# Kernel optimization log

Hardware: AMD Instinct MI355X
Metric: run time of the kernel (lower is better)

The kernel has to match this reference:

```python
import jax, jax.numpy as jnp
import numpy as np

DIM = 384
HEADS = 12
WS = (2, 7, 7)
SS = (1, 3, 3)
B, D, H, W = 4, 8, 56, 56
N = WS[0] * WS[1] * WS[2]  # 98


def _win_part_np(x, ws):
    b, d, h, w, c = x.shape
    x = x.reshape(b, d // ws[0], ws[0], h // ws[1], ws[1], w // ws[2], ws[2], c)
    return x.transpose(0, 1, 3, 5, 2, 4, 6, 7).reshape(-1, ws[0] * ws[1] * ws[2], c)


def setup_inputs() -> dict:
    key = jax.random.key(0)
    ks = jax.random.split(key, 6)
    s = 0.02
    x = jax.random.normal(ks[0], (B, D, H, W, DIM), jnp.float32)
    # relative position index (static int buffer)
    coords = np.stack(np.meshgrid(np.arange(WS[0]), np.arange(WS[1]), np.arange(WS[2]), indexing='ij')).reshape(3, -1)
    rel = (coords[:, :, None] - coords[:, None, :]).transpose(1, 2, 0)
    rel[..., 0] += WS[0] - 1
    rel[..., 1] += WS[1] - 1
    rel[..., 2] += WS[2] - 1
    rel[..., 0] *= (2 * WS[1] - 1) * (2 * WS[2] - 1)
    rel[..., 1] *= 2 * WS[2] - 1
    rel_index = jnp.asarray(rel.sum(-1), jnp.int32)  # [N, N]
    # shifted-window attention mask (standard Swin construction)
    img = np.zeros((1, D, H, W, 1), np.float32)
    cnt = 0
    for dsl in (slice(0, -WS[0]), slice(-WS[0], -SS[0]), slice(-SS[0], None)):
        for hsl in (slice(0, -WS[1]), slice(-WS[1], -SS[1]), slice(-SS[1], None)):
            for wsl in (slice(0, -WS[2]), slice(-WS[2], -SS[2]), slice(-SS[2], None)):
                img[:, dsl, hsl, wsl, :] = cnt
                cnt += 1
    mw = _win_part_np(img, WS).squeeze(-1)  # [nW, N]
    attn_mask = np.where(mw[:, None, :] != mw[:, :, None], -100.0, 0.0).astype(np.float32)
    table_size = (2 * WS[0] - 1) * (2 * WS[1] - 1) * (2 * WS[2] - 1)
    return {
        'x': x,
        'mask': jnp.asarray(attn_mask),
        'rel_table': jax.random.normal(ks[1], (table_size, HEADS), jnp.float32) * s,
        'rel_index': rel_index,
        'qkv_w': jax.random.normal(ks[2], (3 * DIM, DIM), jnp.float32) * s,
        'qkv_b': jnp.zeros((3 * DIM,), jnp.float32),
        'proj_w': jax.random.normal(ks[3], (DIM, DIM), jnp.float32) * s,
        'proj_b': jnp.zeros((DIM,), jnp.float32),
        'g1': jnp.ones((DIM,), jnp.float32), 'b1': jnp.zeros((DIM,), jnp.float32),
        'g2': jnp.ones((DIM,), jnp.float32), 'b2': jnp.zeros((DIM,), jnp.float32),
        'fc1_w': jax.random.normal(ks[4], (DIM, DIM), jnp.float32) * s,
        'fc1_b': jnp.zeros((DIM,), jnp.float32),
        'fc2_w': jax.random.normal(ks[5], (DIM, DIM), jnp.float32) * s,
        'fc2_b': jnp.zeros((DIM,), jnp.float32),
    }


def _ln(x, g, b, eps=1e-5):
    mu = x.mean(-1, keepdims=True)
    var = jnp.mean((x - mu) ** 2, axis=-1, keepdims=True)
    return (x - mu) * jax.lax.rsqrt(var + eps) * g + b


def _window_partition(x, ws):
    b, d, h, w, c = x.shape
    x = x.reshape(b, d // ws[0], ws[0], h // ws[1], ws[1], w // ws[2], ws[2], c)
    return x.transpose(0, 1, 3, 5, 2, 4, 6, 7).reshape(-1, ws[0] * ws[1] * ws[2], c)


def _window_reverse(win, ws, b, d, h, w):
    x = win.reshape(b, d // ws[0], h // ws[1], w // ws[2], ws[0], ws[1], ws[2], -1)
    return x.transpose(0, 1, 4, 2, 5, 3, 6, 7).reshape(b, d, h, w, -1)


def reference(x, mask, rel_table, rel_index, qkv_w, qkv_b, proj_w, proj_b,
              g1, b1, g2, b2, fc1_w, fc1_b, fc2_w, fc2_b):
    shortcut = x
    h = _ln(x, g1, b1)
    b, d, hh, ww, c = h.shape
    # get_window_size: clamp window/shift to input extents (static here)
    ws = [min(WS[i], (d, hh, ww)[i]) for i in range(3)]
    ss = [0 if (d, hh, ww)[i] <= WS[i] else SS[i] for i in range(3)]
    pad = [(ws[i] - (d, hh, ww)[i] % ws[i]) % ws[i] for i in range(3)]
    h = jnp.pad(h, ((0, 0), (0, pad[0]), (0, pad[1]), (0, pad[2]), (0, 0)))
    dp, hp, wp = h.shape[1:4]
    if any(ss):
        h = jnp.roll(h, shift=(-ss[0], -ss[1], -ss[2]), axis=(1, 2, 3))
    xw = _window_partition(h, ws)  # [B_, N, C]
    bw, n, _ = xw.shape
    hd = c // HEADS
    qkv = (xw @ qkv_w.T + qkv_b).reshape(bw, n, 3, HEADS, hd).transpose(2, 0, 3, 1, 4)
    q, k, v = qkv[0], qkv[1], qkv[2]  # [B_, H, N, hd]
    scale = hd ** -0.5
    attn = jnp.einsum('bhnd,bhmd->bhnm', q * scale, k)
    bias = rel_table[rel_index[:n, :n].reshape(-1)].reshape(n, n, HEADS).transpose(2, 0, 1)
    attn = attn + bias[None]
    nW = mask.shape[0]
    attn = attn.reshape(bw // nW, nW, HEADS, n, n) + mask[None, :, None]
    attn = jax.nn.softmax(attn.reshape(bw, HEADS, n, n), axis=-1)
    out = jnp.einsum('bhnm,bhmd->bhnd', attn, v).transpose(0, 2, 1, 3).reshape(bw, n, c)
    out = out @ proj_w.T + proj_b
    out = _window_reverse(out, ws, b, dp, hp, wp)
    if any(ss):
        out = jnp.roll(out, shift=(ss[0], ss[1], ss[2]), axis=(1, 2, 3))
    out = out[:, :d, :hh, :ww, :]
    x1 = shortcut + out
    h2 = _ln(x1, g2, b2)
    mlp = jax.nn.gelu(h2 @ fc1_w.T + fc1_b, approximate=False) @ fc2_w.T + fc2_b
    return x1 + mlp
```

## Files before the change

### kernel.cpp

```cpp
#include <hip/hip_runtime.h>
#include <hip/hip_bf16.h>

#define HEADS 12
#define NWIN 1024
#define NW_MASK 256
#define NTOK 98
#define CDIM 384
#define NROWS (NWIN * NTOK)
#define QKVN (3 * CDIM)
#define PSTR 136
#define LOG2E 1.4426950408889634f
#define SCALE_LOG2E 0.25503486f
#define KSTEPS 12

using u16 = unsigned short;
typedef __attribute__((ext_vector_type(8))) short short8;
typedef __attribute__((ext_vector_type(4))) short s16x4;
typedef __attribute__((ext_vector_type(4))) float f32x4;
typedef __attribute__((ext_vector_type(2))) unsigned u32x2;

__device__ __forceinline__ float b2f(u16 u) { return __uint_as_float(((unsigned)u) << 16); }
__device__ __forceinline__ u16 f2b(float f) {
  unsigned u = __float_as_uint(f);
  u += 0x7FFF + ((u >> 16) & 1);
  return (u16)(u >> 16);
}

__device__ __forceinline__ int tok_of_row(int r) {
  int win = r / NTOK;
  int j   = r - win * NTOK;
  int b   = win >> 8;
  int wl  = win & 255;
  int wd = wl >> 6, wh = (wl >> 3) & 7, ww = wl & 7;
  int od = j / 49; int rem = j - od * 49;
  int oh = rem / 7; int ow = rem - oh * 7;
  int sd = (wd * 2 + od + 1) & 7;
  int sh = wh * 7 + oh + 3; if (sh >= 56) sh -= 56;
  int sw = ww * 7 + ow + 3; if (sw >= 56) sw -= 56;
  return ((b * 8 + sd) * 56 + sh) * 56 + sw;
}

__device__ __forceinline__ int xcd_swz(int bid, int nwg) {
  int q = nwg >> 3, r = nwg & 7;
  int xcd = bid & 7, i = bid >> 3;
  return ((xcd < r) ? xcd * (q + 1) : r * (q + 1) + (xcd - r) * q) + i;
}

__global__ void detect_kernel(const unsigned* __restrict__ g1w, int* __restrict__ flag) {
  if (threadIdx.x == 0 && blockIdx.x == 0)
    flag[0] = (g1w[0] == 0x3F800000u) ? 1 : 0;
}

__device__ __forceinline__ float raw_at(const void* src, size_t j, int isf32) {
  return isf32 ? ((const float*)src)[j] : b2f(((const u16*)src)[j]);
}

struct CvtArgs {
  const void* src[12];
  unsigned off[13];
};
__global__ __launch_bounds__(256) void cvt_all(CvtArgs a, u16* __restrict__ dst,
                                               const int* __restrict__ flag) {
  int i = blockIdx.x * 256 + threadIdx.x;
  if (i >= (int)a.off[12]) return;
  int s = 0;
#pragma unroll
  for (int k = 1; k < 12; ++k) s += (i >= (int)a.off[k]);
  int j = i - (int)a.off[s];
  dst[i] = flag[0] ? f2b(((const float*)a.src[s])[j]) : ((const u16*)a.src[s])[j];
}

template<bool GATHER>
__global__ __launch_bounds__(256) void ln_kernel(const void* __restrict__ in,
                                                 const u16* __restrict__ gam,
                                                 const u16* __restrict__ bet,
                                                 u16* __restrict__ outp,
                                                 const int* __restrict__ flag,
                                                 int maybe_f32) {
  int wrow = blockIdx.x * 4 + (threadIdx.x >> 6);
  int lane = threadIdx.x & 63;
  int isf32 = maybe_f32 ? flag[0] : 0;
  size_t srow = GATHER ? (size_t)tok_of_row(wrow) : (size_t)wrow;
  const u16*   ip16 = (const u16*)in + srow * CDIM;
  const float* ip32 = (const float*)in + srow * CDIM;
  float xv[6]; float s = 0.f, s2 = 0.f;
#pragma unroll
  for (int i = 0; i < 6; ++i) {
    int c = lane + 64 * i;
    xv[i] = isf32 ? ip32[c] : b2f(ip16[c]);
    s += xv[i]; s2 += xv[i] * xv[i];
  }
#pragma unroll
  for (int off = 1; off < 64; off <<= 1) {
    s  += __shfl_xor(s, off);
    s2 += __shfl_xor(s2, off);
  }
  float mu = s * (1.f / CDIM);
  float var = s2 * (1.f / CDIM) - mu * mu;
  float rstd = rsqrtf(var + 1e-5f);
  u16* op = outp + (size_t)wrow * CDIM;
#pragma unroll
  for (int i = 0; i < 6; ++i) {
    int c = lane + 64 * i;
    op[c] = f2b((xv[i] - mu) * rstd * b2f(gam[c]) + b2f(bet[c]));
  }
}

__global__ void bias_kernel(const void* __restrict__ tab, const int* __restrict__ idx,
                            float* __restrict__ biasf, const int* __restrict__ flag) {
  int i = blockIdx.x * 256 + threadIdx.x;
  if (i >= HEADS * NTOK * 100) return;
  int isf32 = flag[0];
  int h = i / (NTOK * 100);
  int rem = i - h * (NTOK * 100);
  int q = rem / 100, t = rem - q * 100;
  biasf[i] = (t < NTOK) ? raw_at(tab, (size_t)idx[q * NTOK + t] * HEADS + h, isf32) * LOG2E : 0.f;
}

__global__ void maskp_kernel(const void* __restrict__ msrc, u16* __restrict__ mdst,
                             const int* __restrict__ flag) {
  int i = blockIdx.x * 256 + threadIdx.x;
  if (i >= NW_MASK * NTOK * 100) return;
  int isf32 = flag[0];
  int w = i / (NTOK * 100);
  int rem = i - w * (NTOK * 100);
  int q = rem / 100, t = rem - q * 100;
  mdst[i] = (t < NTOK) ? f2b(raw_at(msrc, (size_t)(w * NTOK + q) * NTOK + t, isf32) * LOG2E)
                       : (u16)0;
}

__device__ __forceinline__ void gload16(const u16* g, u16* l) {
  __builtin_amdgcn_global_load_lds((const __attribute__((address_space(1))) unsigned*)g,
                                   (__attribute__((address_space(3))) unsigned*)l,
                                   16, 0, 0);
}

template<int EPI>
__global__ __launch_bounds__(256) void gemm_bt(const u16* __restrict__ A, int lda,
                                               const u16* __restrict__ W,
                                               const u16* __restrict__ bias,
                                               int NB, void* __restrict__ outb, int ldo,
                                               const void* __restrict__ aux,
                                               const int* __restrict__ flag) {
  __shared__ __align__(16) u16 lA[2][128 * 32];
  __shared__ __align__(16) u16 lB[2][128 * 32];
  int bid = xcd_swz(blockIdx.x, gridDim.x);
  int mb = bid / NB, nb = bid - mb * NB;
  int row0 = mb * 128, col0 = nb * 128;
  int tid = threadIdx.x;
  int lane = tid & 63;
  int wid = tid >> 6;
  int wr = (wid >> 1) * 64, wc = (wid & 1) * 64;
  f32x4 zero = {0.f, 0.f, 0.f, 0.f};
  f32x4 acc[4][4];
#pragma unroll
  for (int m = 0; m < 4; ++m)
#pragma unroll
    for (int n = 0; n < 4; ++n) acc[m][n] = zero;

  int r0 = tid >> 2, s0 = tid & 3;
  int r1 = 64 + r0;
  int c0 = 8 * (s0 ^ ((r0 >> 1) & 3));
  int c1 = 8 * (s0 ^ ((r1 >> 1) & 3));
  const u16* Ab0 = &A[(size_t)(row0 + r0) * lda + c0];
  const u16* Ab1 = &A[(size_t)(row0 + r1) * lda + c1];
  const u16* Wb0 = &W[(size_t)(col0 + r0) * CDIM + c0];
  const u16* Wb1 = &W[(size_t)(col0 + r1) * CDIM + c1];
  int e0 = tid * 8, e1 = 2048 + tid * 8;
  int g = (lane >> 4) * 8, fr = lane & 15;
  int sw = 8 * ((lane >> 4) ^ ((fr >> 1) & 3));

  gload16(Ab0, &lA[0][e0]);
  gload16(Ab1, &lA[0][e1]);
  gload16(Wb0, &lB[0][e0]);
  gload16(Wb1, &lB[0][e1]);
  __syncthreads();

#pragma unroll
  for (int t = 0; t < KSTEPS; ++t) {
    int cur = t & 1;
    if (t < KSTEPS - 1) {
      int kt = (t + 1) * 32;
      gload16(Ab0 + kt, &lA[cur ^ 1][e0]);
      gload16(Ab1 + kt, &lA[cur ^ 1][e1]);
      gload16(Wb0 + kt, &lB[cur ^ 1][e0]);
      gload16(Wb1 + kt, &lB[cur ^ 1][e1]);
    }
    short8 af[4], bf[4];
#pragma unroll
    for (int m = 0; m < 4; ++m) af[m] = *(const short8*)&lA[cur][(wr + m * 16 + fr) * 32 + sw];
#pragma unroll
    for (int n = 0; n < 4; ++n) bf[n] = *(const short8*)&lB[cur][(wc + n * 16 + fr) * 32 + sw];
#pragma unroll
    for (int m = 0; m < 4; ++m)
#pragma unroll
      for (int n = 0; n < 4; ++n)
        acc[m][n] = __builtin_amdgcn_mfma_f32_16x16x32_bf16(af[m], bf[n], acc[m][n], 0, 0, 0);
    __syncthreads();
  }

  int isf32 = (EPI == 1 || EPI == 3) ? flag[0] : 0;
  int colo = lane & 15;
  int rowo = (lane >> 4) * 4;
  float bv[4];
#pragma unroll
  for (int n = 0; n < 4; ++n) bv[n] = b2f(bias[col0 + wc + n * 16 + colo]);
#pragma unroll
  for (int m = 0; m < 4; ++m) {
#pragma unroll
    for (int r = 0; r < 4; ++r) {
      int gr = row0 + wr + m * 16 + rowo + r;
      int t = (EPI == 1 || EPI == 3) ? tok_of_row(gr) : 0;
#pragma unroll
      for (int n = 0; n < 4; ++n) {
        int gc = col0 + wc + n * 16 + colo;
        float v = acc[m][n][r] + bv[n];
        if (EPI == 0) {
          ((u16*)outb)[(size_t)gr * ldo + gc] = f2b(v);
        } else if (EPI == 1) {
          float xs = isf32 ? ((const float*)aux)[(size_t)t * CDIM + gc]
                           : b2f(((const u16*)aux)[(size_t)t * CDIM + gc]);
          ((u16*)outb)[(size_t)gr * ldo + gc] = f2b(v + xs);
        } else if (EPI == 2) {
          float ge = 0.5f * v * (1.f + erff(v * 0.70710678118654752f));
          ((u16*)outb)[(size_t)gr * ldo + gc] = f2b(ge);
        } else {
          float x1v = b2f(((const u16*)aux)[(size_t)gr * CDIM + gc]);
          float o = v + x1v;
          if (isf32) ((float*)outb)[(size_t)t * CDIM + gc] = o;
          else       ((u16*)outb)[(size_t)t * CDIM + gc] = f2b(o);
        }
      }
    }
  }
}

__global__ __launch_bounds__(256, 3) void attn_mfma(u16* __restrict__ qkv,
                                                    const u16* __restrict__ maskp,
                                                    const float* __restrict__ biasf) {
  __shared__ __align__(16) u16 P4[4][16 * PSTR];
  int wid = threadIdx.x >> 6, lane = threadIdx.x & 63;
  int gh = blockIdx.x * 4 + wid;
  int win = gh / HEADS, hd = gh - win * HEADS;
  int l15 = lane & 15, g = lane >> 4;
  u16* P = P4[wid];
  const size_t base = (size_t)win * NTOK * QKVN + (size_t)hd * 32;
  u16* qp = qkv + base;
  const u16* kp = qkv + base + CDIM;
  const u16* vp = qkv + base + 2 * CDIM;
  const f32x4 zero = {0.f, 0.f, 0.f, 0.f};

  { u32x2 z = {0u, 0u}; *(u32x2*)&P[l15 * PSTR + 112 + 4 * g] = z; }

  short8 kf[7];
#pragma unroll
  for (int n = 0; n < 7; ++n) {
    int tok = n * 16 + l15; if (tok > NTOK - 1) tok = NTOK - 1;
    kf[n] = *(const short8*)&kp[(size_t)tok * QKVN + 8 * g];
  }
  short8 vf[2][4];
#pragma unroll
  for (int kk = 0; kk < 4; ++kk)
#pragma unroll
    for (int i = 0; i < 8; ++i) {
      int tok = 32 * kk + 8 * g + i;
      const u16* vr = vp + (size_t)tok * QKVN + l15;
      u16 v0 = (tok < NTOK) ? vr[0]  : (u16)0;
      u16 v1 = (tok < NTOK) ? vr[16] : (u16)0;
      vf[0][kk][i] = (short)v0;
      vf[1][kk][i] = (short)v1;
    }

  const float* brow = biasf + (size_t)hd * NTOK * 100;
  const u16*   mrow = maskp + (size_t)(win & (NW_MASK - 1)) * NTOK * 100;

  for (int m = 0; m < 7; ++m) {
    int qrow = m * 16 + l15;
    int qr = qrow > NTOK - 1 ? NTOK - 1 : qrow;
    short8 qf = *(const short8*)&qp[(size_t)qr * QKVN + 8 * g];
    f32x4 st[7];
#pragma unroll
    for (int n = 0; n < 7; ++n)
      st[n] = __builtin_amdgcn_mfma_f32_16x16x32_bf16(kf[n], qf, zero, 0, 0, 0);

    float pv[7][4];
    float mx = -1e30f;
#pragma unroll
    for (int n = 0; n < 7; ++n) {
      f32x4 bb = *(const f32x4*)&brow[(size_t)qr * 100 + n * 16 + 4 * g];
      s16x4 mm = *(const s16x4*)&mrow[(size_t)qr * 100 + n * 16 + 4 * g];
#pragma unroll
      for (int r = 0; r < 4; ++r) {
        int tok = n * 16 + 4 * g + r;
        float s = st[n][r] * SCALE_LOG2E + bb[r] + b2f((u16)mm[r]);
        if (tok > NTOK - 1) s = -1e30f;
        pv[n][r] = s;
        mx = fmaxf(mx, s);
      }
    }
    mx = fmaxf(mx, __shfl_xor(mx, 16));
    mx = fmaxf(mx, __shfl_xor(mx, 32));
    float sum = 0.f;
#pragma unroll
    for (int n = 0; n < 7; ++n)
#pragma unroll
      for (int r = 0; r < 4; ++r) {
        float e = exp2f(pv[n][r] - mx);
        pv[n][r] = e; sum += e;
      }
    sum += __shfl_xor(sum, 16);
    sum += __shfl_xor(sum, 32);
    float inv = 1.f / sum;
#pragma unroll
    for (int n = 0; n < 7; ++n) {
      __hip_bfloat162 h0 = __float22bfloat162_rn(make_float2(pv[n][0] * inv, pv[n][1] * inv));
      __hip_bfloat162 h1 = __float22bfloat162_rn(make_float2(pv[n][2] * inv, pv[n][3] * inv));
      u32x2 wv = { *(unsigned*)&h0, *(unsigned*)&h1 };
      *(u32x2*)&P[l15 * PSTR + n * 16 + 4 * g] = wv;
    }
    f32x4 oa0 = zero, oa1 = zero;
#pragma unroll
    for (int kk = 0; kk < 4; ++kk) {
      short8 pf = *(const short8*)&P[l15 * PSTR + kk * 32 + 8 * g];
      oa0 = __builtin_amdgcn_mfma_f32_16x16x32_bf16(pf, vf[0][kk], oa0, 0, 0, 0);
      oa1 = __builtin_amdgcn_mfma_f32_16x16x32_bf16(pf, vf[1][kk], oa1, 0, 0, 0);
    }
#pragma unroll
    for (int r = 0; r < 4; ++r) {
      int row = m * 16 + 4 * g + r;
      if (row < NTOK) {
        qp[(size_t)row * QKVN + l15]      = f2b(oa0[r]);
        qp[(size_t)row * QKVN + 16 + l15] = f2b(oa1[r]);
      }
    }
  }
}

extern "C" void kernel_launch(void* const* d_in, const int* in_sizes, int n_in,
                              void* d_out, int out_size, void* d_ws, size_t ws_size,
                              hipStream_t stream) {
  (void)n_in; (void)out_size; (void)ws_size;
  const void* x    = d_in[0];
  const int* ridx  = (const int*)d_in[3];

  char* ws = (char*)d_ws;
  const size_t SZ_QKV = (size_t)NROWS * QKVN * 2;
  const size_t SZ_MAT = (size_t)NROWS * CDIM * 2;
  const size_t SZ_BIAS = (size_t)HEADS * NTOK * 100 * 4;
  const size_t SZ_MASKP = (size_t)NW_MASK * NTOK * 100 * 2;
  u16* qkv     = (u16*)ws;
  u16* bufA    = (u16*)(ws + SZ_QKV);
  u16* bufX1   = (u16*)(ws + SZ_QKV + SZ_MAT);
  float* biasf = (float*)(ws + SZ_QKV + 2 * SZ_MAT);
  u16* maskp   = (u16*)(ws + SZ_QKV + 2 * SZ_MAT + SZ_BIAS);
  int* flag    = (int*)(ws + SZ_QKV + 2 * SZ_MAT + SZ_BIAS + SZ_MASKP);
  u16* cvt     = (u16*)((char*)flag + 256);

  detect_kernel<<<1, 64, 0, stream>>>((const unsigned*)d_in[8], flag);

  CvtArgs ca;
  unsigned off = 0;
  u16* cp[16];
  for (int k = 0; k < 12; ++k) {
    int i = 4 + k;
    ca.src[k] = d_in[i];
    ca.off[k] = off;
    cp[i] = cvt + off;
    off += (unsigned)in_sizes[i];
  }
  ca.off[12] = off;
  cvt_all<<<(off + 255) / 256, 256, 0, stream>>>(ca, cvt, flag);

  bias_kernel<<<(HEADS * NTOK * 100 + 255) / 256, 256, 0, stream>>>(d_in[2], ridx, biasf, flag);
  maskp_kernel<<<(NW_MASK * NTOK * 100 + 255) / 256, 256, 0, stream>>>(d_in[1], maskp, flag);
  ln_kernel<true><<<NROWS / 4, 256, 0, stream>>>(x, cp[8], cp[9], bufA, flag, 1);
  gemm_bt<0><<<(NROWS / 128) * (QKVN / 128), 256, 0, stream>>>(
      bufA, CDIM, cp[4], cp[5], QKVN / 128, qkv, QKVN, nullptr, flag);
  attn_mfma<<<(NWIN * HEADS) / 4, 256, 0, stream>>>(qkv, maskp, biasf);
  gemm_bt<1><<<(NROWS / 128) * (CDIM / 128), 256, 0, stream>>>(
      qkv, QKVN, cp[6], cp[7], CDIM / 128, bufX1, CDIM, x, flag);
  ln_kernel<false><<<NROWS / 4, 256, 0, stream>>>(bufX1, cp[10], cp[11], bufA, flag, 0);
  u16* fc1out = qkv;
  gemm_bt<2><<<(NROWS / 128) * (CDIM / 128), 256, 0, stream>>>(
      bufA, CDIM, cp[12], cp[13], CDIM / 128, fc1out, CDIM, nullptr, flag);
  gemm_bt<3><<<(NROWS / 128) * (CDIM / 128), 256, 0, stream>>>(
      fc1out, CDIM, cp[14], cp[15], CDIM / 128, d_out, CDIM, bufX1, flag);
}
```

Before: 831.7 us.

## Store QKV head-major so attention reads contiguous per-head tiles

The QKV GEMM epilogue now scatters its output into a [window][q/k/v][head][token][32] layout instead of row-major with a 1152-wide stride. The attention kernel then reads Q, K and V with a 32-element token stride, which gives contiguous 6 KB tiles per head instead of strided 64-byte pieces. Attention output now goes to a separate buffer (bufA) read by the projection GEMM, rather than overwriting Q in place. The cost is a less coalesced GEMM store pattern with extra index arithmetic in the epilogue.

```diff
diff --git a/kernel.cpp b/kernel.cpp
--- a/kernel.cpp
+++ b/kernel.cpp
@@ -211,12 +211,18 @@
     for (int r = 0; r < 4; ++r) {
       int gr = row0 + wr + m * 16 + rowo + r;
       int t = (EPI == 1 || EPI == 3) ? tok_of_row(gr) : 0;
+      int win = 0, tok = 0;
+      if (EPI == 0) { win = gr / NTOK; tok = gr - win * NTOK; }
 #pragma unroll
       for (int n = 0; n < 4; ++n) {
         int gc = col0 + wc + n * 16 + colo;
         float v = acc[m][n][r] + bv[n];
         if (EPI == 0) {
-          ((u16*)outb)[(size_t)gr * ldo + gc] = f2b(v);
+          int cb = col0 + wc + n * 16;
+          int which = cb / 384;
+          int rem = cb - which * 384;
+          int hh = rem >> 5, dd = rem & 31;
+          ((u16*)outb)[((((size_t)win * 3 + which) * HEADS + hh) * NTOK + tok) * 32 + dd + colo] = f2b(v);
         } else if (EPI == 1) {
           float xs = isf32 ? ((const float*)aux)[(size_t)t * CDIM + gc]
                            : b2f(((const u16*)aux)[(size_t)t * CDIM + gc]);
@@ -235,7 +241,8 @@
   }
 }
 
-__global__ __launch_bounds__(256, 3) void attn_mfma(u16* __restrict__ qkv,
+__global__ __launch_bounds__(256, 3) void attn_mfma(const u16* __restrict__ qkvB,
+                                                    u16* __restrict__ obuf,
                                                     const u16* __restrict__ maskp,
                                                     const float* __restrict__ biasf) {
   __shared__ __align__(16) u16 P4[4][16 * PSTR];
@@ -244,10 +251,11 @@
   int win = gh / HEADS, hd = gh - win * HEADS;
   int l15 = lane & 15, g = lane >> 4;
   u16* P = P4[wid];
-  const size_t base = (size_t)win * NTOK * QKVN + (size_t)hd * 32;
-  u16* qp = qkv + base;
-  const u16* kp = qkv + base + CDIM;
-  const u16* vp = qkv + base + 2 * CDIM;
+  const size_t hsz = (size_t)NTOK * 32;
+  const u16* qp = qkvB + ((size_t)(win * 3 + 0) * HEADS + hd) * hsz;
+  const u16* kp = qkvB + ((size_t)(win * 3 + 1) * HEADS + hd) * hsz;
+  const u16* vp = qkvB + ((size_t)(win * 3 + 2) * HEADS + hd) * hsz;
+  u16* op = obuf + ((size_t)win * NTOK) * CDIM + hd * 32;
   const f32x4 zero = {0.f, 0.f, 0.f, 0.f};
 
   { u32x2 z = {0u, 0u}; *(u32x2*)&P[l15 * PSTR + 112 + 4 * g] = z; }
@@ -256,7 +264,7 @@
 #pragma unroll
   for (int n = 0; n < 7; ++n) {
     int tok = n * 16 + l15; if (tok > NTOK - 1) tok = NTOK - 1;
-    kf[n] = *(const short8*)&kp[(size_t)tok * QKVN + 8 * g];
+    kf[n] = *(const short8*)&kp[tok * 32 + 8 * g];
   }
   short8 vf[2][4];
 #pragma unroll
@@ -264,7 +272,7 @@
 #pragma unroll
     for (int i = 0; i < 8; ++i) {
       int tok = 32 * kk + 8 * g + i;
-      const u16* vr = vp + (size_t)tok * QKVN + l15;
+      const u16* vr = vp + tok * 32 + l15;
       u16 v0 = (tok < NTOK) ? vr[0]  : (u16)0;
       u16 v1 = (tok < NTOK) ? vr[16] : (u16)0;
       vf[0][kk][i] = (short)v0;
@@ -277,7 +285,7 @@
   for (int m = 0; m < 7; ++m) {
     int qrow = m * 16 + l15;
     int qr = qrow > NTOK - 1 ? NTOK - 1 : qrow;
-    short8 qf = *(const short8*)&qp[(size_t)qr * QKVN + 8 * g];
+    short8 qf = *(const short8*)&qp[qr * 32 + 8 * g];
     f32x4 st[7];
 #pragma unroll
     for (int n = 0; n < 7; ++n)
@@ -329,8 +337,8 @@
     for (int r = 0; r < 4; ++r) {
       int row = m * 16 + 4 * g + r;
       if (row < NTOK) {
-        qp[(size_t)row * QKVN + l15]      = f2b(oa0[r]);
-        qp[(size_t)row * QKVN + 16 + l15] = f2b(oa1[r]);
+        op[(size_t)row * CDIM + l15]      = f2b(oa0[r]);
+        op[(size_t)row * CDIM + 16 + l15] = f2b(oa1[r]);
       }
     }
   }
@@ -348,7 +356,7 @@
   const size_t SZ_MAT = (size_t)NROWS * CDIM * 2;
   const size_t SZ_BIAS = (size_t)HEADS * NTOK * 100 * 4;
   const size_t SZ_MASKP = (size_t)NW_MASK * NTOK * 100 * 2;
-  u16* qkv     = (u16*)ws;
+  u16* qkvB    = (u16*)ws;
   u16* bufA    = (u16*)(ws + SZ_QKV);
   u16* bufX1   = (u16*)(ws + SZ_QKV + SZ_MAT);
   float* biasf = (float*)(ws + SZ_QKV + 2 * SZ_MAT);
@@ -375,12 +383,12 @@
   maskp_kernel<<<(NW_MASK * NTOK * 100 + 255) / 256, 256, 0, stream>>>(d_in[1], maskp, flag);
   ln_kernel<true><<<NROWS / 4, 256, 0, stream>>>(x, cp[8], cp[9], bufA, flag, 1);
   gemm_bt<0><<<(NROWS / 128) * (QKVN / 128), 256, 0, stream>>>(
-      bufA, CDIM, cp[4], cp[5], QKVN / 128, qkv, QKVN, nullptr, flag);
-  attn_mfma<<<(NWIN * HEADS) / 4, 256, 0, stream>>>(qkv, maskp, biasf);
+      bufA, CDIM, cp[4], cp[5], QKVN / 128, qkvB, 0, nullptr, flag);
+  attn_mfma<<<(NWIN * HEADS) / 4, 256, 0, stream>>>(qkvB, bufA, maskp, biasf);
   gemm_bt<1><<<(NROWS / 128) * (CDIM / 128), 256, 0, stream>>>(
-      qkv, QKVN, cp[6], cp[7], CDIM / 128, bufX1, CDIM, x, flag);
+      bufA, CDIM, cp[6], cp[7], CDIM / 128, bufX1, CDIM, x, flag);
   ln_kernel<false><<<NROWS / 4, 256, 0, stream>>>(bufX1, cp[10], cp[11], bufA, flag, 0);
-  u16* fc1out = qkv;
+  u16* fc1out = qkvB;
   gemm_bt<2><<<(NROWS / 128) * (CDIM / 128), 256, 0, stream>>>(
       bufA, CDIM, cp[12], cp[13], CDIM / 128, fc1out, CDIM, nullptr, flag);
   gemm_bt<3><<<(NROWS / 128) * (CDIM / 128), 256, 0, stream>>>(
```

New measurement: 848.7 us. 2.0% more time.
